# Optimization experiments

Measured on AMD Instinct MI355X. Metric: run time of the kernel, lower is better.

## Reference

```python
import jax, jax.numpy as jnp
import numpy as np

B, L, H = 64, 512, 400          # batch, seq_len, encoder hidden (HeadSentinel(400))
EN, EL, NLAB = 256, 128, 128    # edge-node dim, edge-label hidden, num head_tags


def setup_inputs():
    key = jax.random.key(0)
    ks = jax.random.split(key, 16)
    g = lambda k, shape, s=0.05: jax.random.normal(k, shape, jnp.float32) * s
    return dict(
        memory_bank=jax.random.normal(ks[0], (B, L, H), jnp.float32),
        edge_heads=jax.random.randint(ks[1], (B, L), 0, L + 1, jnp.int32),
        edge_labels=jax.random.randint(ks[2], (B, L), 0, NLAB, jnp.int32),
        corefs=jax.random.randint(ks[3], (B, L), 0, L, jnp.int32),
        mask=jnp.ones((B, L), jnp.int32),
        sentinel=g(ks[4], (H,)),
        W_enh=g(ks[5], (H, EN)), b_enh=jnp.zeros((EN,), jnp.float32),
        W_enm=g(ks[6], (H, EN)), b_enm=jnp.zeros((EN,), jnp.float32),
        W_elh=g(ks[7], (H, EL)), b_elh=jnp.zeros((EL,), jnp.float32),
        W_elm=g(ks[8], (H, EL)), b_elm=jnp.zeros((EL,), jnp.float32),
        ba_U=g(ks[9], (EN, EN)), ba_Wd=g(ks[10], (EN,)), ba_We=g(ks[11], (EN,)),
        ba_b=jnp.zeros((), jnp.float32),
        lbl_U=g(ks[12], (NLAB, EL, EL)), lbl_Wl=g(ks[13], (NLAB, EL)),
        lbl_Wr=g(ks[14], (NLAB, EL)), lbl_b=jnp.zeros((NLAB,), jnp.float32),
    )


def _label_scores(elh_sel, elm, lbl_U, lbl_Wl, lbl_Wr, lbl_b):
    # Bilinear label scorer: [B, L1, NLAB]
    return (jnp.einsum('bld,nde,ble->bln', elh_sel, lbl_U, elm)
            + elh_sel @ lbl_Wl.T + elm @ lbl_Wr.T + lbl_b)


def reference(memory_bank, edge_heads, edge_labels, corefs, mask, sentinel,
              W_enh, b_enh, W_enm, b_enm, W_elh, b_elh, W_elm, b_elm,
              ba_U, ba_Wd, ba_We, ba_b, lbl_U, lbl_Wl, lbl_Wr, lbl_b):
    elu = jax.nn.elu
    Bsz = memory_bank.shape[0]
    # ---- add head sentinel (mask/heads/labels get a leading zero column) ----
    mb = jnp.concatenate([jnp.broadcast_to(sentinel, (Bsz, 1, sentinel.shape[0])), memory_bank], 1)
    z = jnp.zeros((Bsz, 1), jnp.int32)
    heads1 = jnp.concatenate([z, edge_heads], 1)    # [B, L1]
    labels1 = jnp.concatenate([z, edge_labels], 1)  # [B, L1]
    mask1 = jnp.concatenate([z, mask], 1)           # [B, L1]
    L1 = mb.shape[1]
    # ---- encode (Dropout is identity at inference) ----
    enh = elu(mb @ W_enh + b_enh)
    enm = elu(mb @ W_enm + b_enm)
    elh = elu(mb @ W_elh + b_elh)
    elm = elu(mb @ W_elm + b_elm)
    # ---- biaffine edge-node scores: s[b, head, mod] ----
    node_scores = (jnp.einsum('bhd,de,bme->bhm', enh, ba_U, enm)
                   + (enh @ ba_Wd)[:, :, None] + (enm @ ba_We)[:, None, :] + ba_b)
    # ---- loss ----
    mask2 = (mask1[:, :, None] + mask1[:, None, :]).astype(jnp.float32)
    node_ll = jax.nn.log_softmax(node_scores + jnp.log(mask2 + 1e-45), axis=1)
    elh_gold = jnp.take_along_axis(elh, heads1[:, :, None], axis=1)  # gather_nd(create_indices)
    lbl_ll = jax.nn.log_softmax(_label_scores(elh_gold, elm, lbl_U, lbl_Wl, lbl_Wr, lbl_b), axis=2)
    gold_node_ll = jnp.take_along_axis(node_ll, heads1[:, None, :], axis=1)[:, 0, :]  # ll[b, head[b,m], m]
    gold_lbl_ll = jnp.take_along_axis(lbl_ll, labels1[:, :, None], axis=2)[:, :, 0]   # ll[b, m, label[b,m]]
    node_nll = -jnp.sum(gold_node_ll[:, 1:])
    label_nll = -jnp.sum(gold_lbl_ll[:, 1:])
    # ---- decode ----
    dec = node_scores + jnp.diag(jnp.full((L1,), -jnp.inf))
    mm = (1.0 - mask1.astype(jnp.float32)) * (-1e8)
    dec = dec + mm[:, :, None] + mm[:, None, :]
    pred_heads = jnp.argmax(dec, axis=1)                              # [B, L1]
    elh_pred = jnp.take_along_axis(elh, pred_heads[:, :, None], axis=1)
    pred_lbl = jnp.max(_label_scores(elh_pred, elm, lbl_U, lbl_Wl, lbl_Wr, lbl_b), axis=2)
    return (pred_heads[:, 1:].astype(jnp.float32), pred_lbl[:, 1:],
            labels1.astype(jnp.float32), node_nll, label_nll)
```

## Files before the change

### kernel.cpp

```cpp
#include <hip/hip_runtime.h>
#include <hip/hip_bf16.h>

#define BB 64
#define LLEN 512
#define HH 400
#define L1 513
#define TT 32832
#define NE 768
#define KP 16640
#define PHW 4160
#define KPAD 416

typedef __attribute__((ext_vector_type(4))) float f32x4;
typedef __attribute__((ext_vector_type(8))) short bf16x8;
typedef unsigned int u32;
typedef __attribute__((address_space(1))) const u32* gptr_t;
typedef __attribute__((address_space(3))) u32* sptr_t;

__device__ inline unsigned short f2bf(float x){
  unsigned u = __float_as_uint(x);
  unsigned r = (u + 0x7fffu + ((u >> 16) & 1u)) >> 16;
  return (unsigned short)r;
}
__device__ inline unsigned cvtpk(float a, float b){
  unsigned r;
  asm("v_cvt_pk_bf16_f32 %0, %1, %2" : "=v"(r) : "v"(a), "v"(b));
  return r;
}
__device__ inline float bf2f(unsigned short h){
  return __uint_as_float(((unsigned)h) << 16);
}

__global__ __launch_bounds__(256) void k_init(const int* eh, const int* el, float* out,
                                              int* idx, int* labbuf, const float* bab,
                                              float* dvec, float* evec){
  int t = blockIdx.x*256 + threadIdx.x;
  if (t < TT){
    int b = t / L1, m = t - b*L1;
    int lab = m ? el[b*LLEN + m - 1] : 0;
    int hd  = m ? eh[b*LLEN + m - 1] : 0;
    out[65536 + t] = (float)lab;
    labbuf[t] = lab;
    idx[t] = b*L1 + hd;
    dvec[t] = bab[0];
    evec[t] = 0.f;
  }
  if (blockIdx.x == 0 && threadIdx.x < 2) out[98368 + threadIdx.x] = 0.f;
}

__global__ __launch_bounds__(256) void k_wcat(const float* Wenh,const float* benh,
    const float* Wenm,const float* benm,const float* Welh,const float* belh,
    const float* Welm,const float* belm, unsigned short* WH, unsigned short* WL,
    float* bcat){
  int g = blockIdx.x*256 + threadIdx.x;
  if (g < NE*KPAD){
    int n = g / KPAD, k = g - n*KPAD;
    float v = 0.f;
    if (k < HH){
      if (n < 256) v = Wenh[k*256 + n];
      else if (n < 512) v = Wenm[k*256 + n - 256];
      else if (n < 640) v = Welh[k*128 + n - 512];
      else v = Welm[k*128 + n - 640];
    }
    unsigned short h = f2bf(v);
    WH[g] = h;
    WL[g] = f2bf(v - bf2f(h));
  }
  if (g < NE){
    float v;
    if (g < 256) v = benh[g];
    else if (g < 512) v = benm[g - 256];
    else if (g < 640) v = belh[g - 512];
    else v = belm[g - 640];
    bcat[g] = v;
  }
}

__global__ __launch_bounds__(256) void k_wu(const float* baU, unsigned short* UH,
    unsigned short* UL){
  int g = blockIdx.x*256 + threadIdx.x;
  int n = g >> 8, k = g & 255;
  float v = baU[k*256 + n];
  unsigned short h = f2bf(v);
  UH[g] = h;
  UL[g] = f2bf(v - bf2f(h));
}

__global__ __launch_bounds__(256) void k_wtt(const float* lblU, const float* Wl,
    const float* Wr, unsigned short* WtTp){
  int n = blockIdx.y;
  int kp = blockIdx.x*256 + threadIdx.x;
  if (kp >= KP) return;
  int p = kp / PHW; int q2 = kp - p*PHW; int dd = q2 >> 5; int j = q2 & 31; int e = p*32 + j;
  float v;
  if (dd < 128) v = lblU[(size_t)n*16384 + dd*128 + e];
  else if (dd == 128) v = Wl[n*128 + e];
  else v = Wr[n*128 + e];
  WtTp[(size_t)n*KP + kp] = f2bf(v);
}

__global__ __launch_bounds__(512) void k_encm(const float* mb, const float* sent,
    const unsigned short* WH, const unsigned short* WL, const float* bcat,
    const float* Wd, const float* We, float* dvec, float* evec, float* E){
  __shared__ __align__(16) unsigned char Bst[2][2][8192];
  int tid = threadIdx.x, w = tid >> 6, lane = tid & 63, c = lane & 15, q = lane >> 4;
  int tb0 = blockIdx.x*256 + w*32;
  int n0 = blockIdx.y*128;

  const float* ap[2];
  #pragma unroll
  for (int ms = 0; ms < 2; ms++){
    int row = tb0 + ms*16 + c;
    const float* p = sent;
    if (row < TT){
      int br = row / L1, mr = row - br*L1;
      if (mr) p = mb + (size_t)(br*LLEN + mr - 1)*HH;
    }
    ap[ms] = p;
  }

  int f = tid;
  int bn = ((f >> 6) << 4) + (f & 15);
  int bkq = (f >> 4) & 3;
  const char* srcH = (const char*)WH + (size_t)(n0 + bn)*(KPAD*2) + bkq*16;
  const char* srcL = (const char*)WL + (size_t)(n0 + bn)*(KPAD*2) + bkq*16;
  auto stageB = [&](int s){
    __builtin_amdgcn_global_load_lds((gptr_t)(srcH + (size_t)s*64),
        (sptr_t)(&Bst[s & 1][0][f*16]), 16, 0, 0);
    __builtin_amdgcn_global_load_lds((gptr_t)(srcL + (size_t)s*64),
        (sptr_t)(&Bst[s & 1][1][f*16]), 16, 0, 0);
  };

  float4 a0[2], a1[2];
  auto loadA = [&](int s){
    #pragma unroll
    for (int ms = 0; ms < 2; ms++){
      int k = s*32 + q*8;
      float4 v0 = make_float4(0.f,0.f,0.f,0.f), v1 = v0;
      if (k < HH){ v0 = *(const float4*)(ap[ms] + k); v1 = *(const float4*)(ap[ms] + k + 4); }
      a0[ms] = v0; a1[ms] = v1;
    }
  };
  stageB(0);
  loadA(0);

  f32x4 acc[2][8];
  #pragma unroll
  for (int ms = 0; ms < 2; ms++)
    #pragma unroll
    for (int ns = 0; ns < 8; ns++){ acc[ms][ns][0]=0.f; acc[ms][ns][1]=0.f; acc[ms][ns][2]=0.f; acc[ms][ns][3]=0.f; }

  for (int s = 0; s < 13; s++){
    asm volatile("s_waitcnt vmcnt(0)" ::: "memory");
    __builtin_amdgcn_sched_barrier(0);
    __builtin_amdgcn_s_barrier();
    __builtin_amdgcn_sched_barrier(0);
    if (s + 1 < 13) stageB(s + 1);
    bf16x8 Ah[2], Al[2];
    #pragma unroll
    for (int ms = 0; ms < 2; ms++){
      float v[8] = {a0[ms].x,a0[ms].y,a0[ms].z,a0[ms].w,a1[ms].x,a1[ms].y,a1[ms].z,a1[ms].w};
      union { unsigned u[4]; bf16x8 b; } uh, ul;
      float r[8];
      #pragma unroll
      for (int j = 0; j < 4; j++){
        unsigned h = cvtpk(v[2*j], v[2*j+1]);
        uh.u[j] = h;
        r[2*j]   = v[2*j]   - __uint_as_float((h & 0xffffu) << 16);
        r[2*j+1] = v[2*j+1] - __uint_as_float((h >> 16) << 16);
      }
      #pragma unroll
      for (int j = 0; j < 4; j++) ul.u[j] = cvtpk(r[2*j], r[2*j+1]);
      Ah[ms] = uh.b; Al[ms] = ul.b;
    }
    if (s + 1 < 13) loadA(s + 1);
    const char* bh = (const char*)&Bst[s & 1][0][0];
    const char* bl = (const char*)&Bst[s & 1][1][0];
    #pragma unroll
    for (int ns = 0; ns < 8; ns++){
      bf16x8 BH = *(const bf16x8*)(bh + ns*1024 + lane*16);
      bf16x8 BL = *(const bf16x8*)(bl + ns*1024 + lane*16);
      #pragma unroll
      for (int ms = 0; ms < 2; ms++){
        acc[ms][ns] = __builtin_amdgcn_mfma_f32_16x16x32_bf16(Ah[ms], BH, acc[ms][ns], 0, 0, 0);
        acc[ms][ns] = __builtin_amdgcn_mfma_f32_16x16x32_bf16(Ah[ms], BL, acc[ms][ns], 0, 0, 0);
        acc[ms][ns] = __builtin_amdgcn_mfma_f32_16x16x32_bf16(Al[ms], BH, acc[ms][ns], 0, 0, 0);
      }
    }
  }

  int yb = blockIdx.y;
  bool isD = yb < 2, isE = (yb >= 2 && yb < 4);
  float wv[8];
  if (isD){
    #pragma unroll
    for (int ns = 0; ns < 8; ns++) wv[ns] = Wd[n0 + ns*16 + c];
  } else if (isE){
    #pragma unroll
    for (int ns = 0; ns < 8; ns++) wv[ns] = We[n0 - 256 + ns*16 + c];
  }
  float bvv[8];
  #pragma unroll
  for (int ns = 0; ns < 8; ns++) bvv[ns] = bcat[n0 + ns*16 + c];
  #pragma unroll
  for (int ms = 0; ms < 2; ms++){
    #pragma unroll
    for (int i = 0; i < 4; i++){
      int row = tb0 + ms*16 + 4*q + i;
      float p = 0.f;
      if (row < TT){
        #pragma unroll
        for (int ns = 0; ns < 8; ns++){
          float t = acc[ms][ns][i] + bvv[ns];
          float e = t > 0.f ? t : expm1f(t);
          E[(size_t)row*NE + n0 + ns*16 + c] = e;
          if (isD || isE) p += e * wv[ns];
        }
      }
      if (isD || isE){
        #pragma unroll
        for (int o = 1; o < 16; o <<= 1) p += __shfl_xor(p, o, 64);
        if (c == 0 && row < TT) atomicAdd((isD ? dvec : evec) + row, p);
      }
    }
  }
}

__global__ __launch_bounds__(256) void k_t1m(const float* E, const unsigned short* UH,
    const unsigned short* UL, float* T1){
  __shared__ __align__(16) unsigned char Bst[2][2][8192];
  int tid = threadIdx.x, w = tid >> 6, lane = tid & 63, c = lane & 15, q = lane >> 4;
  int tb0 = blockIdx.x*128 + w*32;
  int n0 = blockIdx.y*128;

  const float* ap[2];
  #pragma unroll
  for (int ms = 0; ms < 2; ms++){
    int row = tb0 + ms*16 + c;
    ap[ms] = E + (size_t)(row < TT ? row : 0)*NE;
  }

  auto stageB = [&](int s){
    #pragma unroll
    for (int i = 0; i < 2; i++){
      int f = i*256 + tid;
      int n = n0 + ((f >> 6) << 4) + (f & 15);
      int kq = (f >> 4) & 3;
      __builtin_amdgcn_global_load_lds((gptr_t)((const char*)UH + (size_t)n*512 + (size_t)s*64 + kq*16),
          (sptr_t)(&Bst[s & 1][0][f*16]), 16, 0, 0);
      __builtin_amdgcn_global_load_lds((gptr_t)((const char*)UL + (size_t)n*512 + (size_t)s*64 + kq*16),
          (sptr_t)(&Bst[s & 1][1][f*16]), 16, 0, 0);
    }
  };

  float4 a0[2], a1[2];
  auto loadA = [&](int s){
    #pragma unroll
    for (int ms = 0; ms < 2; ms++){
      int k = s*32 + q*8;
      a0[ms] = *(const float4*)(ap[ms] + k);
      a1[ms] = *(const float4*)(ap[ms] + k + 4);
    }
  };
  stageB(0);
  loadA(0);

  f32x4 acc[2][8];
  #pragma unroll
  for (int ms = 0; ms < 2; ms++)
    #pragma unroll
    for (int ns = 0; ns < 8; ns++){ acc[ms][ns][0]=0.f; acc[ms][ns][1]=0.f; acc[ms][ns][2]=0.f; acc[ms][ns][3]=0.f; }

  for (int s = 0; s < 8; s++){
    asm volatile("s_waitcnt vmcnt(0)" ::: "memory");
    __builtin_amdgcn_sched_barrier(0);
    __builtin_amdgcn_s_barrier();
    __builtin_amdgcn_sched_barrier(0);
    if (s + 1 < 8) stageB(s + 1);
    bf16x8 Ah[2], Al[2];
    #pragma unroll
    for (int ms = 0; ms < 2; ms++){
      float v[8] = {a0[ms].x,a0[ms].y,a0[ms].z,a0[ms].w,a1[ms].x,a1[ms].y,a1[ms].z,a1[ms].w};
      union { unsigned u[4]; bf16x8 b; } uh, ul;
      float r[8];
      #pragma unroll
      for (int j = 0; j < 4; j++){
        unsigned h = cvtpk(v[2*j], v[2*j+1]);
        uh.u[j] = h;
        r[2*j]   = v[2*j]   - __uint_as_float((h & 0xffffu) << 16);
        r[2*j+1] = v[2*j+1] - __uint_as_float((h >> 16) << 16);
      }
      #pragma unroll
      for (int j = 0; j < 4; j++) ul.u[j] = cvtpk(r[2*j], r[2*j+1]);
      Ah[ms] = uh.b; Al[ms] = ul.b;
    }
    if (s + 1 < 8) loadA(s + 1);
    const char* bh = (const char*)&Bst[s & 1][0][0];
    const char* bl = (const char*)&Bst[s & 1][1][0];
    #pragma unroll
    for (int ns = 0; ns < 8; ns++){
      bf16x8 BH = *(const bf16x8*)(bh + ns*1024 + lane*16);
      bf16x8 BL = *(const bf16x8*)(bl + ns*1024 + lane*16);
      #pragma unroll
      for (int ms = 0; ms < 2; ms++){
        acc[ms][ns] = __builtin_amdgcn_mfma_f32_16x16x32_bf16(Ah[ms], BH, acc[ms][ns], 0, 0, 0);
        acc[ms][ns] = __builtin_amdgcn_mfma_f32_16x16x32_bf16(Ah[ms], BL, acc[ms][ns], 0, 0, 0);
        acc[ms][ns] = __builtin_amdgcn_mfma_f32_16x16x32_bf16(Al[ms], BH, acc[ms][ns], 0, 0, 0);
      }
    }
  }

  #pragma unroll
  for (int ms = 0; ms < 2; ms++){
    #pragma unroll
    for (int i = 0; i < 4; i++){
      int row = tb0 + ms*16 + 4*q + i;
      if (row < TT){
        #pragma unroll
        for (int ns = 0; ns < 8; ns++)
          T1[(size_t)row*256 + n0 + ns*16 + c] = acc[ms][ns][i];
      }
    }
  }
}

__global__ __launch_bounds__(256) void k_nsm(const float* T1, const float* E,
    const float* dvec, const float* evec, float* ST){
  __shared__ __align__(16) unsigned char Bst[2][2][8192];
  int tid = threadIdx.x, w = tid >> 6, lane = tid & 63, c = lane & 15, q = lane >> 4;
  int b = blockIdx.y;
  int tm = blockIdx.x / 5, tn = blockIdx.x - tm*5;
  int Mb = tm*128, n0 = tn*128;
  int tb0 = Mb + w*32;

  const float* ap[2];
  #pragma unroll
  for (int ms = 0; ms < 2; ms++){
    int h = tb0 + ms*16 + c;
    int hc = h < L1 ? h : L1 - 1;
    ap[ms] = T1 + ((size_t)b*L1 + hc)*256;
  }

  auto stageB = [&](int s, int buf){
    int k0 = s*32;
    #pragma unroll
    for (int i = 0; i < 2; i++){
      int f = i*256 + tid;
      int mc = n0 + ((f >> 6) << 4) + (f & 15);
      int kq = (f >> 4) & 3;
      int mcc = mc < L1 ? mc : L1 - 1;
      const float* src = E + ((size_t)b*L1 + mcc)*NE + 256 + k0 + kq*8;
      float4 v0 = *(const float4*)src;
      float4 v1 = *(const float4*)(src + 4);
      float v[8] = {v0.x,v0.y,v0.z,v0.w,v1.x,v1.y,v1.z,v1.w};
      union { unsigned u[4]; uint4 u4; } uh, ul;
      float r[8];
      #pragma unroll
      for (int j = 0; j < 4; j++){
        unsigned h = cvtpk(v[2*j], v[2*j+1]);
        uh.u[j] = h;
        r[2*j]   = v[2*j]   - __uint_as_float((h & 0xffffu) << 16);
        r[2*j+1] = v[2*j+1] - __uint_as_float((h >> 16) << 16);
      }
      #pragma unroll
      for (int j = 0; j < 4; j++) ul.u[j] = cvtpk(r[2*j], r[2*j+1]);
      *(uint4*)&Bst[buf][0][f*16] = uh.u4;
      *(uint4*)&Bst[buf][1][f*16] = ul.u4;
    }
  };

  float4 a0[2], a1[2];
  auto loadA = [&](int s){
    #pragma unroll
    for (int ms = 0; ms < 2; ms++){
      int k = s*32 + q*8;
      a0[ms] = *(const float4*)(ap[ms] + k);
      a1[ms] = *(const float4*)(ap[ms] + k + 4);
    }
  };

  stageB(0, 0);
  loadA(0);

  f32x4 acc[2][8];
  #pragma unroll
  for (int ms = 0; ms < 2; ms++)
    #pragma unroll
    for (int ns = 0; ns < 8; ns++){ acc[ms][ns][0]=0.f; acc[ms][ns][1]=0.f; acc[ms][ns][2]=0.f; acc[ms][ns][3]=0.f; }

  __syncthreads();

  for (int s = 0; s < 8; s++){
    if (s + 1 < 8) stageB(s + 1, (s + 1) & 1);
    bf16x8 Ah[2], Al[2];
    #pragma unroll
    for (int ms = 0; ms < 2; ms++){
      float v[8] = {a0[ms].x,a0[ms].y,a0[ms].z,a0[ms].w,a1[ms].x,a1[ms].y,a1[ms].z,a1[ms].w};
      union { unsigned u[4]; bf16x8 b; } uh, ul;
      float r[8];
      #pragma unroll
      for (int j = 0; j < 4; j++){
        unsigned h = cvtpk(v[2*j], v[2*j+1]);
        uh.u[j] = h;
        r[2*j]   = v[2*j]   - __uint_as_float((h & 0xffffu) << 16);
        r[2*j+1] = v[2*j+1] - __uint_as_float((h >> 16) << 16);
      }
      #pragma unroll
      for (int j = 0; j < 4; j++) ul.u[j] = cvtpk(r[2*j], r[2*j+1]);
      Ah[ms] = uh.b; Al[ms] = ul.b;
    }
    if (s + 1 < 8) loadA(s + 1);
    const char* bh = (const char*)&Bst[s & 1][0][0];
    const char* bl = (const char*)&Bst[s & 1][1][0];
    #pragma unroll
    for (int ns = 0; ns < 8; ns++){
      bf16x8 BH = *(const bf16x8*)(bh + ns*1024 + lane*16);
      bf16x8 BL = *(const bf16x8*)(bl + ns*1024 + lane*16);
      #pragma unroll
      for (int ms = 0; ms < 2; ms++){
        acc[ms][ns] = __builtin_amdgcn_mfma_f32_16x16x32_bf16(Ah[ms], BH, acc[ms][ns], 0, 0, 0);
        acc[ms][ns] = __builtin_amdgcn_mfma_f32_16x16x32_bf16(Ah[ms], BL, acc[ms][ns], 0, 0, 0);
        acc[ms][ns] = __builtin_amdgcn_mfma_f32_16x16x32_bf16(Al[ms], BH, acc[ms][ns], 0, 0, 0);
      }
    }
    __syncthreads();
  }

  float er[8];
  #pragma unroll
  for (int ns = 0; ns < 8; ns++){
    int m = n0 + ns*16 + c;
    er[ns] = (m < L1) ? evec[b*L1 + m] : 0.f;
  }
  float* STb = ST + (size_t)b*L1*L1;
  #pragma unroll
  for (int ms = 0; ms < 2; ms++){
    int hb = tb0 + ms*16 + 4*q;
    if (hb < L1){
      bool full = (hb + 3 < L1);
      float dv[4];
      if (full){
        float4 d4 = *(const float4*)&dvec[b*L1 + hb];
        dv[0]=d4.x; dv[1]=d4.y; dv[2]=d4.z; dv[3]=d4.w;
      } else {
        #pragma unroll
        for (int i = 0; i < 4; i++) dv[i] = (hb + i < L1) ? dvec[b*L1 + hb + i] : 0.f;
      }
      #pragma unroll
      for (int ns = 0; ns < 8; ns++){
        int m = n0 + ns*16 + c;
        if (m < L1){
          f32x4 o;
          #pragma unroll
          for (int i = 0; i < 4; i++) o[i] = acc[ms][ns][i] + dv[i] + er[ns];
          if (full) *(f32x4*)&STb[(size_t)m*L1 + hb] = o;
          else {
            #pragma unroll
            for (int i = 0; i < 4; i++) if (hb + i < L1) STb[(size_t)m*L1 + hb + i] = o[i];
          }
        }
      }
    }
  }
}

__global__ __launch_bounds__(256) void k_nodecol(const float* ST, const int* eh,
    const int* mask, float* out, int* idx){
  int b = blockIdx.y;
  int tid = threadIdx.x, w = tid >> 6, lane = tid & 63;
  __shared__ float msk[L1];
  __shared__ float npart[4];
  for (int h = tid; h < L1; h += 256) msk[h] = h ? (float)mask[b*LLEN + h - 1] : 0.f;
  __syncthreads();
  int m = blockIdx.x*4 + w;
  bool valid = m < L1; int mc = valid ? m : (L1-1);
  float maskm = msk[mc];
  int gold = 0; if (valid && m) gold = eh[b*LLEN + m - 1];
  const float* Sm = ST + ((size_t)b*L1 + mc)*L1;
  float Mx = -3.4e38f, Smm = 0.f, G = 0.f, Bv = -3.4e38f; int Bh = 0;
  #pragma unroll
  for (int k = 0; k < 9; k++){
    int h = lane + 64*k;
    if (h < L1){
      float s = Sm[h];
      float adj = s + ((msk[h] + maskm) > 1.5f ? 0.69314718055994531f : 0.f);
      float nm = fmaxf(Mx, adj);
      Smm = Smm * expf(Mx - nm) + expf(adj - nm);
      Mx = nm;
      if (h == gold) G = adj;
      float dv = (h == m) ? -3.4e38f : (s + (msk[h] > 0.5f ? 0.f : -1e8f));
      if (dv > Bv){ Bv = dv; Bh = h; }
    }
  }
  for (int o = 1; o < 64; o <<= 1){
    float M2 = __shfl_xor(Mx, o, 64), S2 = __shfl_xor(Smm, o, 64);
    float nm = fmaxf(Mx, M2);
    Smm = Smm*expf(Mx - nm) + S2*expf(M2 - nm); Mx = nm;
    G += __shfl_xor(G, o, 64);
    float B2 = __shfl_xor(Bv, o, 64); int H2 = __shfl_xor(Bh, o, 64);
    if (B2 > Bv || (B2 == Bv && H2 < Bh)){ Bv = B2; Bh = H2; }
  }
  float nll = 0.f;
  if (valid && m >= 1) nll = (Mx + logf(Smm)) - G;
  if (lane == 0){
    npart[w] = nll;
    if (valid){
      idx[TT + b*L1 + m] = b*L1 + Bh;
      if (m >= 1) out[b*LLEN + m - 1] = (float)Bh;
    }
  }
  __syncthreads();
  if (tid == 0){
    float s4 = npart[0] + npart[1] + npart[2] + npart[3];
    if (s4 != 0.f) atomicAdd(out + 98368, s4);
  }
}

__global__ __launch_bounds__(512, 1) void k_label(const float* E, const unsigned short* WtTp,
    const int* idx, const int* labbuf, const float* lblb, float* out){
  __shared__ __align__(16) unsigned char Bst[8*8192];
  __shared__ __align__(16) unsigned int xls[256*65];
  int tid = threadIdx.x;
  int w = tid >> 6, lane = tid & 63, c = lane & 15, q = lane >> 4;
  int wgrp = w & 3, khalf = w >> 2;
  int bx = blockIdx.x;
  bool pred = bx >= 128;
  int q0 = (bx & 127) * 256;
  int ibase = pred ? TT : 0;

  const char* gW = (const char*)WtTp;
  int f = tid;
  int bn = ((f >> 6) << 4) + (f & 15);
  int bkq = (f >> 4) & 3;
  const char* bsrc0 = gW + (size_t)bn*(KP*2) + (size_t)bkq*16;
  unsigned char* BbA = Bst;
  unsigned char* BbB = Bst + 4*8192;
  auto stage2 = [&](int s){
    __builtin_amdgcn_global_load_lds((gptr_t)(bsrc0 + (size_t)s*64),
        (sptr_t)(BbA + (s & 3)*8192 + f*16), 16, 0, 0);
    __builtin_amdgcn_global_load_lds((gptr_t)(bsrc0 + (size_t)(260 + s)*64),
        (sptr_t)(BbB + (s & 3)*8192 + f*16), 16, 0, 0);
  };
  stage2(0); stage2(1);

  {
    int tok = tid >> 1, half = tid & 1;
    int qq = q0 + tok;
    int trow = (qq >> 9)*L1 + (qq & 511) + 1;
    int g = idx[ibase + trow];
    const float* xr = E + (size_t)g*NE + 512 + half*64;
    unsigned* dstx = &xls[tok*65 + half*32];
    #pragma unroll
    for (int j = 0; j < 16; j++){
      float4 v = *(const float4*)(xr + j*4);
      dstx[2*j]   = cvtpk(v.x, v.y);
      dstx[2*j+1] = cvtpk(v.z, v.w);
    }
  }

  const float *yvb[4], *xvb[4];
  int tokl[4];
  #pragma unroll
  for (int ms = 0; ms < 4; ms++){
    int tl = (wgrp*4 + ms)*16 + c;
    tokl[ms] = tl;
    int qq = q0 + tl;
    int trow = (qq >> 9)*L1 + (qq & 511) + 1;
    int g = idx[ibase + trow];
    yvb[ms] = E + (size_t)trow*NE + 640 + 8*q;
    xvb[ms] = E + (size_t)g*NE + 512 + 8*q;
  }
  f32x4 acc[4][8];
  #pragma unroll
  for (int ms = 0; ms < 4; ms++)
    #pragma unroll
    for (int ns = 0; ns < 8; ns++){ acc[ms][ns][0]=0.f; acc[ms][ns][1]=0.f; acc[ms][ns][2]=0.f; acc[ms][ns][3]=0.f; }

  __syncthreads();

  const unsigned short* xsh = (const unsigned short*)xls;
  float xs0[4], xs1[4];
  #pragma unroll
  for (int ms = 0; ms < 4; ms++){
    xs0[ms] = bf2f(xsh[tokl[ms]*130]);
    xs1[ms] = bf2f(xsh[tokl[ms]*130 + 1]);
  }

  float yreg[4][8];
  for (int u = 0; u < 130; u++){
    if (u) { asm volatile("s_waitcnt vmcnt(0)" ::: "memory"); }
    __builtin_amdgcn_sched_barrier(0);
    __builtin_amdgcn_s_barrier();
    __builtin_amdgcn_sched_barrier(0);
    if (2*u + 2 < 260){ stage2(2*u + 2); stage2(2*u + 3); }
    int ph = (u >= 65);
    int d0 = 2*u - ph*130;
    if (d0 == 0){
      int e0 = (khalf*2 + ph) * 32;
      #pragma unroll
      for (int ms = 0; ms < 4; ms++){
        float4 v0 = *(const float4*)(yvb[ms] + e0);
        float4 v1 = *(const float4*)(yvb[ms] + e0 + 4);
        yreg[ms][0]=v0.x; yreg[ms][1]=v0.y; yreg[ms][2]=v0.z; yreg[ms][3]=v0.w;
        yreg[ms][4]=v1.x; yreg[ms][5]=v1.y; yreg[ms][6]=v1.z; yreg[ms][7]=v1.w;
      }
    }
    bf16x8 afr0[4], afr1[4];
    if (d0 < 128){
      #pragma unroll
      for (int ms = 0; ms < 4; ms++){
        float a0 = xs0[ms], a1 = xs1[ms];
        union { unsigned u[4]; bf16x8 v; } u0, u1;
        u0.u[0] = cvtpk(a0*yreg[ms][0], a0*yreg[ms][1]);
        u0.u[1] = cvtpk(a0*yreg[ms][2], a0*yreg[ms][3]);
        u0.u[2] = cvtpk(a0*yreg[ms][4], a0*yreg[ms][5]);
        u0.u[3] = cvtpk(a0*yreg[ms][6], a0*yreg[ms][7]);
        u1.u[0] = cvtpk(a1*yreg[ms][0], a1*yreg[ms][1]);
        u1.u[1] = cvtpk(a1*yreg[ms][2], a1*yreg[ms][3]);
        u1.u[2] = cvtpk(a1*yreg[ms][4], a1*yreg[ms][5]);
        u1.u[3] = cvtpk(a1*yreg[ms][6], a1*yreg[ms][7]);
        afr0[ms] = u0.v; afr1[ms] = u1.v;
      }
    } else {
      int e0 = (khalf*2 + ph) * 32;
      #pragma unroll
      for (int ms = 0; ms < 4; ms++){
        float4 u0f = *(const float4*)(xvb[ms] + e0);
        float4 u1f = *(const float4*)(xvb[ms] + e0 + 4);
        union { unsigned u[4]; bf16x8 v; } ux, uy;
        ux.u[0]=cvtpk(u0f.x,u0f.y); ux.u[1]=cvtpk(u0f.z,u0f.w);
        ux.u[2]=cvtpk(u1f.x,u1f.y); ux.u[3]=cvtpk(u1f.z,u1f.w);
        uy.u[0]=cvtpk(yreg[ms][0],yreg[ms][1]); uy.u[1]=cvtpk(yreg[ms][2],yreg[ms][3]);
        uy.u[2]=cvtpk(yreg[ms][4],yreg[ms][5]); uy.u[3]=cvtpk(yreg[ms][6],yreg[ms][7]);
        afr0[ms] = ux.v; afr1[ms] = uy.v;
      }
    }
    {
      int nd0 = 2*(u + 1) - ((u + 1 >= 65) ? 130 : 0);
      if (nd0 >= 128) nd0 = 0;
      #pragma unroll
      for (int ms = 0; ms < 4; ms++){
        xs0[ms] = bf2f(xsh[tokl[ms]*130 + nd0]);
        xs1[ms] = bf2f(xsh[tokl[ms]*130 + nd0 + 1]);
      }
    }
    const char* hb = (const char*)(khalf ? BbB : BbA);
    const char* bs0 = hb + ((2*u) & 3)*8192;
    const char* bs1 = hb + ((2*u + 1) & 3)*8192;
    __builtin_amdgcn_s_setprio(1);
    #pragma unroll
    for (int ns = 0; ns < 8; ns++){
      bf16x8 bfr0 = *(const bf16x8*)(bs0 + ns*1024 + lane*16);
      bf16x8 bfr1 = *(const bf16x8*)(bs1 + ns*1024 + lane*16);
      #pragma unroll
      for (int ms = 0; ms < 4; ms++){
        acc[ms][ns] = __builtin_amdgcn_mfma_f32_16x16x32_bf16(afr0[ms], bfr0, acc[ms][ns], 0, 0, 0);
        acc[ms][ns] = __builtin_amdgcn_mfma_f32_16x16x32_bf16(afr1[ms], bfr1, acc[ms][ns], 0, 0, 0);
      }
    }
    __builtin_amdgcn_s_setprio(0);
  }

  __syncthreads();
  float* cmb = (float*)xls;
  #pragma unroll
  for (int ms = 0; ms < 4; ms++){
    if (khalf == 1){
      #pragma unroll
      for (int ns = 0; ns < 8; ns++)
        *(f32x4*)&cmb[((wgrp*64 + lane)*8 + ((ns + lane) & 7))*4] = acc[ms][ns];
    }
    __syncthreads();
    if (khalf == 0){
      #pragma unroll
      for (int ns = 0; ns < 8; ns++){
        f32x4 t = *(const f32x4*)&cmb[((wgrp*64 + lane)*8 + ((ns + lane) & 7))*4];
        acc[ms][ns][0] += t[0]; acc[ms][ns][1] += t[1];
        acc[ms][ns][2] += t[2]; acc[ms][ns][3] += t[3];
      }
    }
    __syncthreads();
  }
  if (khalf == 1) return;

  float bv[8];
  #pragma unroll
  for (int ns = 0; ns < 8; ns++) bv[ns] = lblb[ns*16 + c];
  float part = 0.f;
  #pragma unroll
  for (int ms = 0; ms < 4; ms++){
    int tb = (wgrp*4 + ms)*16 + 4*q;
    float mx[4] = {-3.4e38f, -3.4e38f, -3.4e38f, -3.4e38f};
    #pragma unroll
    for (int ns = 0; ns < 8; ns++)
      #pragma unroll
      for (int i = 0; i < 4; i++){
        float v = acc[ms][ns][i] + bv[ns];
        mx[i] = fmaxf(mx[i], v);
      }
    #pragma unroll
    for (int o = 1; o < 16; o <<= 1)
      #pragma unroll
      for (int i = 0; i < 4; i++) mx[i] = fmaxf(mx[i], __shfl_xor(mx[i], o, 64));
    if (!pred){
      int lab[4];
      #pragma unroll
      for (int i = 0; i < 4; i++){
        int qq = q0 + tb + i;
        int trow = (qq >> 9)*L1 + (qq & 511) + 1;
        lab[i] = labbuf[trow];
      }
      float se[4] = {0.f,0.f,0.f,0.f}, gp[4] = {0.f,0.f,0.f,0.f};
      #pragma unroll
      for (int ns = 0; ns < 8; ns++)
        #pragma unroll
        for (int i = 0; i < 4; i++){
          float v = acc[ms][ns][i] + bv[ns];
          se[i] += expf(v - mx[i]);
          if (ns*16 + c == lab[i]) gp[i] += v;
        }
      #pragma unroll
      for (int o = 1; o < 16; o <<= 1)
        #pragma unroll
        for (int i = 0; i < 4; i++){ se[i] += __shfl_xor(se[i], o, 64); gp[i] += __shfl_xor(gp[i], o, 64); }
      if (c == 0){
        #pragma unroll
        for (int i = 0; i < 4; i++) part += mx[i] + logf(se[i]) - gp[i];
      }
    } else {
      if (c == 0){
        #pragma unroll
        for (int i = 0; i < 4; i++)
          out[32768 + q0 + tb + i] = mx[i];
      }
    }
  }
  if (!pred){
    for (int o = 1; o < 64; o <<= 1) part += __shfl_xor(part, o, 64);
    if (lane == 0) atomicAdd(out + 98369, part);
  }
}

extern "C" void kernel_launch(void* const* d_in, const int* in_sizes, int n_in,
                              void* d_out, int out_size, void* d_ws, size_t ws_size,
                              hipStream_t stream){
  const float* memory_bank = (const float*)d_in[0];
  const int* edge_heads = (const int*)d_in[1];
  const int* edge_labels = (const int*)d_in[2];
  const int* mask = (const int*)d_in[4];
  const float* sentinel = (const float*)d_in[5];
  const float* W_enh = (const float*)d_in[6];  const float* b_enh = (const float*)d_in[7];
  const float* W_enm = (const float*)d_in[8];  const float* b_enm = (const float*)d_in[9];
  const float* W_elh = (const float*)d_in[10]; const float* b_elh = (const float*)d_in[11];
  const float* W_elm = (const float*)d_in[12]; const float* b_elm = (const float*)d_in[13];
  const float* ba_U = (const float*)d_in[14];  const float* ba_Wd = (const float*)d_in[15];
  const float* ba_We = (const float*)d_in[16]; const float* ba_b = (const float*)d_in[17];
  const float* lbl_U = (const float*)d_in[18]; const float* lbl_Wl = (const float*)d_in[19];
  const float* lbl_Wr = (const float*)d_in[20]; const float* lbl_b = (const float*)d_in[21];
  float* out = (float*)d_out;

  char* wsc = (char*)d_ws;
  size_t o = 0;
  auto alloc = [&](size_t n){ o = (o + 255) & ~(size_t)255; void* pp = wsc + o; o += n; return pp; };
  float* E     = (float*)alloc((size_t)TT*NE*4);
  float* T1    = (float*)alloc((size_t)TT*256*4);
  float* ST    = (float*)alloc((size_t)BB*L1*L1*4);
  unsigned short* WH = (unsigned short*)alloc((size_t)NE*KPAD*2);
  unsigned short* WL = (unsigned short*)alloc((size_t)NE*KPAD*2);
  unsigned short* UH = (unsigned short*)alloc((size_t)256*256*2);
  unsigned short* UL = (unsigned short*)alloc((size_t)256*256*2);
  float* bcat  = (float*)alloc((size_t)NE*4);
  unsigned short* WtTp = (unsigned short*)alloc((size_t)128*KP*2);
  float* dvec  = (float*)alloc((size_t)TT*4);
  float* evec  = (float*)alloc((size_t)TT*4);
  int*   idx   = (int*)alloc((size_t)2*TT*4);
  int*   labbuf= (int*)alloc((size_t)TT*4);

  k_init<<<dim3(129), 256, 0, stream>>>(edge_heads, edge_labels, out, idx, labbuf, ba_b, dvec, evec);
  k_wcat<<<dim3(1248), 256, 0, stream>>>(W_enh, b_enh, W_enm, b_enm, W_elh, b_elh, W_elm, b_elm, WH, WL, bcat);
  k_wu<<<dim3(256), 256, 0, stream>>>(ba_U, UH, UL);
  k_wtt<<<dim3(65, 128), 256, 0, stream>>>(lbl_U, lbl_Wl, lbl_Wr, WtTp);
  k_encm<<<dim3(129, 6), 512, 0, stream>>>(memory_bank, sentinel, WH, WL, bcat, ba_Wd, ba_We, dvec, evec, E);
  k_t1m<<<dim3(257, 2), 256, 0, stream>>>(E, UH, UL, T1);
  k_nsm<<<dim3(25, 64), 256, 0, stream>>>(T1, E, dvec, evec, ST);
  k_nodecol<<<dim3(129, 64), 256, 0, stream>>>(ST, edge_heads, mask, out, idx);
  k_label<<<dim3(256), 512, 0, stream>>>(E, WtTp, idx, labbuf, lbl_b, out);
}
```

Baseline: 769.2 us.

## Split d/e vector reduction into separate kernel and swap nsm operand roles

The Wd/We dot products and their atomicAdd reductions are removed from the encoder GEMM epilogue. A new k_vecs kernel recomputes dvec/evec from E with one wavefront per token, which also takes over the initialisation formerly done in k_init. The k_nsm GEMM now uses E (modifier features) as the A operand and T1 as B, and its stores change from 4-wide vector writes to per-element coalesced writes along h. The s_setprio hints around the label kernel's MFMA loop are dropped. The split removes atomics and epilogue work from the encoder, at the cost of an extra kernel launch and another full read of half of E.

```diff
diff --git a/kernel.cpp b/kernel.cpp
--- a/kernel.cpp
+++ b/kernel.cpp
@@ -32,8 +32,7 @@
 }
 
 __global__ __launch_bounds__(256) void k_init(const int* eh, const int* el, float* out,
-                                              int* idx, int* labbuf, const float* bab,
-                                              float* dvec, float* evec){
+                                              int* idx, int* labbuf){
   int t = blockIdx.x*256 + threadIdx.x;
   if (t < TT){
     int b = t / L1, m = t - b*L1;
@@ -42,8 +41,6 @@
     out[65536 + t] = (float)lab;
     labbuf[t] = lab;
     idx[t] = b*L1 + hd;
-    dvec[t] = bab[0];
-    evec[t] = 0.f;
   }
   if (blockIdx.x == 0 && threadIdx.x < 2) out[98368 + threadIdx.x] = 0.f;
 }
@@ -100,8 +97,7 @@
 }
 
 __global__ __launch_bounds__(512) void k_encm(const float* mb, const float* sent,
-    const unsigned short* WH, const unsigned short* WL, const float* bcat,
-    const float* Wd, const float* We, float* dvec, float* evec, float* E){
+    const unsigned short* WH, const unsigned short* WL, const float* bcat, float* E){
   __shared__ __align__(16) unsigned char Bst[2][2][8192];
   int tid = threadIdx.x, w = tid >> 6, lane = tid & 63, c = lane & 15, q = lane >> 4;
   int tb0 = blockIdx.x*256 + w*32;
@@ -189,16 +185,6 @@
     }
   }
 
-  int yb = blockIdx.y;
-  bool isD = yb < 2, isE = (yb >= 2 && yb < 4);
-  float wv[8];
-  if (isD){
-    #pragma unroll
-    for (int ns = 0; ns < 8; ns++) wv[ns] = Wd[n0 + ns*16 + c];
-  } else if (isE){
-    #pragma unroll
-    for (int ns = 0; ns < 8; ns++) wv[ns] = We[n0 - 256 + ns*16 + c];
-  }
   float bvv[8];
   #pragma unroll
   for (int ns = 0; ns < 8; ns++) bvv[ns] = bcat[n0 + ns*16 + c];
@@ -207,20 +193,12 @@
     #pragma unroll
     for (int i = 0; i < 4; i++){
       int row = tb0 + ms*16 + 4*q + i;
-      float p = 0.f;
       if (row < TT){
         #pragma unroll
         for (int ns = 0; ns < 8; ns++){
           float t = acc[ms][ns][i] + bvv[ns];
-          float e = t > 0.f ? t : expm1f(t);
-          E[(size_t)row*NE + n0 + ns*16 + c] = e;
-          if (isD || isE) p += e * wv[ns];
+          E[(size_t)row*NE + n0 + ns*16 + c] = t > 0.f ? t : expm1f(t);
         }
-      }
-      if (isD || isE){
-        #pragma unroll
-        for (int o = 1; o < 16; o <<= 1) p += __shfl_xor(p, o, 64);
-        if (c == 0 && row < TT) atomicAdd((isD ? dvec : evec) + row, p);
       }
     }
   }
@@ -324,21 +302,33 @@
   }
 }
 
+__global__ __launch_bounds__(256) void k_vecs(const float* E, const float* Wd,
+    const float* We, const float* bab, float* dvec, float* evec){
+  int w = threadIdx.x >> 6, lane = threadIdx.x & 63;
+  int t = blockIdx.x*4 + w;
+  const float* enh = E + (size_t)t*NE;
+  const float* enm = enh + 256;
+  float sd = 0.f, se = 0.f;
+  for (int l = lane; l < 256; l += 64){ sd += enh[l]*Wd[l]; se += enm[l]*We[l]; }
+  for (int o = 1; o < 64; o <<= 1){ sd += __shfl_xor(sd, o, 64); se += __shfl_xor(se, o, 64); }
+  if (lane == 0){ dvec[t] = sd + bab[0]; evec[t] = se; }
+}
+
 __global__ __launch_bounds__(256) void k_nsm(const float* T1, const float* E,
     const float* dvec, const float* evec, float* ST){
   __shared__ __align__(16) unsigned char Bst[2][2][8192];
   int tid = threadIdx.x, w = tid >> 6, lane = tid & 63, c = lane & 15, q = lane >> 4;
   int b = blockIdx.y;
   int tm = blockIdx.x / 5, tn = blockIdx.x - tm*5;
-  int Mb = tm*128, n0 = tn*128;
+  int Mb = tm*128, Hb = tn*128;
   int tb0 = Mb + w*32;
 
   const float* ap[2];
   #pragma unroll
   for (int ms = 0; ms < 2; ms++){
-    int h = tb0 + ms*16 + c;
-    int hc = h < L1 ? h : L1 - 1;
-    ap[ms] = T1 + ((size_t)b*L1 + hc)*256;
+    int m = tb0 + ms*16 + c;
+    int mc = m < L1 ? m : L1 - 1;
+    ap[ms] = E + ((size_t)b*L1 + mc)*NE + 256;
   }
 
   auto stageB = [&](int s, int buf){
@@ -346,10 +336,10 @@
     #pragma unroll
     for (int i = 0; i < 2; i++){
       int f = i*256 + tid;
-      int mc = n0 + ((f >> 6) << 4) + (f & 15);
+      int h = Hb + ((f >> 6) << 4) + (f & 15);
       int kq = (f >> 4) & 3;
-      int mcc = mc < L1 ? mc : L1 - 1;
-      const float* src = E + ((size_t)b*L1 + mcc)*NE + 256 + k0 + kq*8;
+      int hc = h < L1 ? h : L1 - 1;
+      const float* src = T1 + ((size_t)b*L1 + hc)*256 + k0 + kq*8;
       float4 v0 = *(const float4*)src;
       float4 v1 = *(const float4*)(src + 4);
       float v[8] = {v0.x,v0.y,v0.z,v0.w,v1.x,v1.y,v1.z,v1.w};
@@ -357,10 +347,10 @@
       float r[8];
       #pragma unroll
       for (int j = 0; j < 4; j++){
-        unsigned h = cvtpk(v[2*j], v[2*j+1]);
-        uh.u[j] = h;
-        r[2*j]   = v[2*j]   - __uint_as_float((h & 0xffffu) << 16);
-        r[2*j+1] = v[2*j+1] - __uint_as_float((h >> 16) << 16);
+        unsigned h2 = cvtpk(v[2*j], v[2*j+1]);
+        uh.u[j] = h2;
+        r[2*j]   = v[2*j]   - __uint_as_float((h2 & 0xffffu) << 16);
+        r[2*j+1] = v[2*j+1] - __uint_as_float((h2 >> 16) << 16);
       }
       #pragma unroll
       for (int j = 0; j < 4; j++) ul.u[j] = cvtpk(r[2*j], r[2*j+1]);
@@ -426,38 +416,24 @@
     __syncthreads();
   }
 
-  float er[8];
+  float hr[8];
   #pragma unroll
   for (int ns = 0; ns < 8; ns++){
-    int m = n0 + ns*16 + c;
-    er[ns] = (m < L1) ? evec[b*L1 + m] : 0.f;
+    int h = Hb + ns*16 + c;
+    hr[ns] = (h < L1) ? dvec[b*L1 + h] : 0.f;
   }
   float* STb = ST + (size_t)b*L1*L1;
   #pragma unroll
   for (int ms = 0; ms < 2; ms++){
-    int hb = tb0 + ms*16 + 4*q;
-    if (hb < L1){
-      bool full = (hb + 3 < L1);
-      float dv[4];
-      if (full){
-        float4 d4 = *(const float4*)&dvec[b*L1 + hb];
-        dv[0]=d4.x; dv[1]=d4.y; dv[2]=d4.z; dv[3]=d4.w;
-      } else {
+    #pragma unroll
+    for (int i = 0; i < 4; i++){
+      int m = tb0 + ms*16 + 4*q + i;
+      if (m < L1){
+        float ev = evec[b*L1 + m];
         #pragma unroll
-        for (int i = 0; i < 4; i++) dv[i] = (hb + i < L1) ? dvec[b*L1 + hb + i] : 0.f;
-      }
-      #pragma unroll
-      for (int ns = 0; ns < 8; ns++){
-        int m = n0 + ns*16 + c;
-        if (m < L1){
-          f32x4 o;
-          #pragma unroll
-          for (int i = 0; i < 4; i++) o[i] = acc[ms][ns][i] + dv[i] + er[ns];
-          if (full) *(f32x4*)&STb[(size_t)m*L1 + hb] = o;
-          else {
-            #pragma unroll
-            for (int i = 0; i < 4; i++) if (hb + i < L1) STb[(size_t)m*L1 + hb + i] = o[i];
-          }
+        for (int ns = 0; ns < 8; ns++){
+          int h = Hb + ns*16 + c;
+          if (h < L1) STb[(size_t)m*L1 + h] = acc[ms][ns][i] + ev + hr[ns];
         }
       }
     }
@@ -647,7 +623,6 @@
     const char* hb = (const char*)(khalf ? BbB : BbA);
     const char* bs0 = hb + ((2*u) & 3)*8192;
     const char* bs1 = hb + ((2*u + 1) & 3)*8192;
-    __builtin_amdgcn_s_setprio(1);
     #pragma unroll
     for (int ns = 0; ns < 8; ns++){
       bf16x8 bfr0 = *(const bf16x8*)(bs0 + ns*1024 + lane*16);
@@ -658,7 +633,6 @@
         acc[ms][ns] = __builtin_amdgcn_mfma_f32_16x16x32_bf16(afr1[ms], bfr1, acc[ms][ns], 0, 0, 0);
       }
     }
-    __builtin_amdgcn_s_setprio(0);
   }
 
   __syncthreads();
@@ -776,12 +750,13 @@
   int*   idx   = (int*)alloc((size_t)2*TT*4);
   int*   labbuf= (int*)alloc((size_t)TT*4);
 
-  k_init<<<dim3(129), 256, 0, stream>>>(edge_heads, edge_labels, out, idx, labbuf, ba_b, dvec, evec);
+  k_init<<<dim3(129), 256, 0, stream>>>(edge_heads, edge_labels, out, idx, labbuf);
   k_wcat<<<dim3(1248), 256, 0, stream>>>(W_enh, b_enh, W_enm, b_enm, W_elh, b_elh, W_elm, b_elm, WH, WL, bcat);
   k_wu<<<dim3(256), 256, 0, stream>>>(ba_U, UH, UL);
   k_wtt<<<dim3(65, 128), 256, 0, stream>>>(lbl_U, lbl_Wl, lbl_Wr, WtTp);
-  k_encm<<<dim3(129, 6), 512, 0, stream>>>(memory_bank, sentinel, WH, WL, bcat, ba_Wd, ba_We, dvec, evec, E);
+  k_encm<<<dim3(129, 6), 512, 0, stream>>>(memory_bank, sentinel, WH, WL, bcat, E);
   k_t1m<<<dim3(257, 2), 256, 0, stream>>>(E, UH, UL, T1);
+  k_vecs<<<dim3(8208), 256, 0, stream>>>(E, ba_Wd, ba_We, ba_b, dvec, evec);
   k_nsm<<<dim3(25, 64), 256, 0, stream>>>(T1, E, dvec, evec, ST);
   k_nodecol<<<dim3(129, 64), 256, 0, stream>>>(ST, edge_heads, mask, out, idx);
   k_label<<<dim3(256), 512, 0, stream>>>(E, WtTp, idx, labbuf, lbl_b, out);
```

New measurement: 755.8 us. Within noise of the previous version (-1.7%).
